# Kernel tuning notes

Hardware: AMD Instinct MI355X
Metric: run time of the kernel (lower is better)

Reference implementation:

```python
import jax, jax.numpy as jnp
import numpy as np

B, N, E = 8, 4096, 8190
V, H, OUT = 256, 128, 128


def setup_inputs() -> dict:
    key = jax.random.key(0)
    ks = jax.random.split(key, 7)
    return {
        "type_ids": jax.random.randint(ks[0], (B, N), 0, V),
        "edges": jax.random.randint(ks[1], (B, E, 2), 0, N),
        "emb": jax.random.normal(ks[2], (V, H), jnp.float32) * 0.02,
        "w1": jax.random.normal(ks[3], (H, H), jnp.float32) * (1.0 / np.sqrt(H)),
        "b1": jax.random.normal(ks[4], (H,), jnp.float32) * 0.01,
        "w2": jax.random.normal(ks[5], (OUT, H), jnp.float32) * (1.0 / np.sqrt(H)),
        "b2": jax.random.normal(ks[6], (OUT,), jnp.float32) * 0.01,
    }


def reference(type_ids, edges, emb, w1, b1, w2, b2):
    # X: [B, N, H] embedded node types
    X = emb[type_ids]
    b_idx = jnp.broadcast_to(jnp.arange(type_ids.shape[0])[:, None], edges.shape[:2])
    # dense adjacency, set (not add) like torch adj[i, j] = 1.0; then + I
    adj = jnp.zeros((type_ids.shape[0], N, N), X.dtype)
    adj = adj.at[b_idx, edges[..., 0], edges[..., 1]].set(1.0)
    adj = adj + jnp.eye(N, dtype=X.dtype)
    # symmetric degree normalization: A = D^-1/2 (adj) D^-1/2
    deg = adj.sum(axis=-1)
    dis = jnp.maximum(deg, 1.0) ** -0.5  # deg.clamp(min=1.0) ** -0.5
    A = dis[:, :, None] * adj * dis[:, None, :]
    # two-layer GCN (torch Linear: x @ W.T + b)
    h = jax.nn.relu(jnp.einsum("bnm,bmh->bnh", A, X) @ w1.T + b1)
    z = jnp.einsum("bnm,bmh->bnh", A, h) @ w2.T + b2
    zbar = z.mean(axis=1)  # per-graph mean pool -> [B, OUT]
    # F.normalize(dim=-1), eps=1e-12
    norm = jnp.maximum(jnp.linalg.norm(zbar, axis=-1, keepdims=True), 1e-12)
    return zbar / norm
```

## Files before the change

### kernel.cpp

```cpp
#include <hip/hip_runtime.h>
#include <hip/hip_bf16.h>
#include <stdint.h>

#define BB 8
#define NN 4096
#define NE 8190
#define VV 256
#define HH 128
#define WPR 64
#define MAXD 32
#define SLICES 64
#define RPB 8

__global__ void k_scatter(const int* __restrict__ edges,
                          unsigned long long* __restrict__ bits,
                          int* __restrict__ outdeg, int* __restrict__ indeg,
                          unsigned short* __restrict__ outl,
                          unsigned short* __restrict__ inl) {
    int idx = blockIdx.x * blockDim.x + threadIdx.x;
    if (idx >= BB * NE) return;
    int b = idx / NE;
    int src = edges[idx * 2 + 0];
    int dst = edges[idx * 2 + 1];
    int row = b * NN + src;
    unsigned long long m = 1ull << (dst & 63);
    unsigned long long old = atomicOr(&bits[(size_t)row * WPR + (dst >> 6)], m);
    if (!(old & m)) {
        int po = atomicAdd(&outdeg[row], 1);
        if (po < MAXD) outl[(size_t)row * MAXD + po] = (unsigned short)dst;
        int col = b * NN + dst;
        int pi = atomicAdd(&indeg[col], 1);
        if (pi < MAXD) inl[(size_t)col * MAXD + pi] = (unsigned short)src;
    }
}

__global__ void k_embw1(const float* __restrict__ emb,
                        const float* __restrict__ w1,
                        float* __restrict__ embw1) {
    __shared__ float er[HH];
    int v = blockIdx.x, o = threadIdx.x;
    er[o] = emb[v * HH + o];
    __syncthreads();
    float acc = 0.f;
#pragma unroll 8
    for (int k = 0; k < HH; k++) acc += er[k] * w1[o * HH + k];
    embw1[v * HH + o] = acc;
}

__global__ void k_fused(const int* __restrict__ type_ids,
                        const float* __restrict__ embw1,
                        const int* __restrict__ outdeg,
                        const int* __restrict__ indeg,
                        const unsigned short* __restrict__ outl,
                        const unsigned short* __restrict__ inl,
                        const float* __restrict__ b1,
                        float* __restrict__ p) {
    __shared__ float djs[MAXD];
    __shared__ int   tjs[MAXD];
    __shared__ float s_sh;
    int t = threadIdx.x;
    int blk = blockIdx.x;
    int base = blk * RPB;
    int b = base >> 12;
    float b1t = b1[t];
    float psum = 0.f;

    for (int r = 0; r < RPB; r++) {
        int row = base + r;
        int mo = min(outdeg[row], MAXD);
        int mi = min(indeg[row], MAXD);
        if (t < mo) {
            int gj = b * NN + (int)outl[(size_t)row * MAXD + t];
            djs[t] = rsqrtf((float)(outdeg[gj] + 1));
            tjs[t] = type_ids[gj];
        }
        float sloc = 0.f;
        if (t < mi) {
            int gu = b * NN + (int)inl[(size_t)row * MAXD + t];
            sloc = rsqrtf((float)(outdeg[gu] + 1));
        }
        if (t < 64) {
#pragma unroll
            for (int off = 16; off >= 1; off >>= 1)
                sloc += __shfl_down(sloc, off, 32);
            if (t == 0) s_sh = sloc;
        }
        __syncthreads();
        float dis_i = rsqrtf((float)(outdeg[row] + 1));
        int ti = type_ids[row];
        float acc = dis_i * embw1[ti * HH + t];
        for (int q = 0; q < mo; q++)
            acc += djs[q] * embw1[tjs[q] * HH + t];
        float h = fmaxf(dis_i * acc + b1t, 0.f);
        float c = dis_i * (s_sh + dis_i);
        psum += c * h;
        __syncthreads();
    }
    int slice = blk & (SLICES - 1);
    atomicAdd(&p[((size_t)b * SLICES + slice) * HH + t], psum);
}

__global__ void k_final(const float* __restrict__ p,
                        const float* __restrict__ w2,
                        const float* __restrict__ b2,
                        float* __restrict__ out) {
    __shared__ float pl[HH];
    __shared__ float red[HH];
    int b = blockIdx.x, o = threadIdx.x;
    float accp = 0.f;
#pragma unroll 8
    for (int sct = 0; sct < SLICES; sct++)
        accp += p[((size_t)b * SLICES + sct) * HH + o];
    pl[o] = accp * (1.0f / (float)NN);
    __syncthreads();
    float acc = b2[o];
#pragma unroll 8
    for (int k = 0; k < HH; k++) acc += pl[k] * w2[o * HH + k];
    red[o] = acc * acc;
    __syncthreads();
    for (int stride = 64; stride > 0; stride >>= 1) {
        if (o < stride) red[o] += red[o + stride];
        __syncthreads();
    }
    float denom = fmaxf(sqrtf(red[0]), 1e-12f);
    out[b * HH + o] = acc / denom;
}

extern "C" void kernel_launch(void* const* d_in, const int* in_sizes, int n_in,
                              void* d_out, int out_size, void* d_ws, size_t ws_size,
                              hipStream_t stream) {
    const int*   type_ids = (const int*)d_in[0];
    const int*   edges    = (const int*)d_in[1];
    const float* emb      = (const float*)d_in[2];
    const float* w1       = (const float*)d_in[3];
    const float* b1       = (const float*)d_in[4];
    const float* w2       = (const float*)d_in[5];
    const float* b2       = (const float*)d_in[6];
    float* out = (float*)d_out;

    char* ws = (char*)d_ws;
    unsigned long long* bits = (unsigned long long*)ws;
    size_t off = (size_t)BB * NN * WPR * 8;
    int* outdeg = (int*)(ws + off);          off += (size_t)BB * NN * 4;
    int* indeg  = (int*)(ws + off);          off += (size_t)BB * NN * 4;
    float* p    = (float*)(ws + off);        off += (size_t)BB * SLICES * HH * 4;
    size_t zero_bytes = off;
    unsigned short* outl = (unsigned short*)(ws + off); off += (size_t)BB * NN * MAXD * 2;
    unsigned short* inl  = (unsigned short*)(ws + off); off += (size_t)BB * NN * MAXD * 2;
    float* embw1 = (float*)(ws + off);

    hipMemsetAsync(ws, 0, zero_bytes, stream);

    k_scatter<<<(BB * NE + 255) / 256, 256, 0, stream>>>(edges, bits, outdeg,
                                                         indeg, outl, inl);
    k_embw1<<<VV, HH, 0, stream>>>(emb, w1, embw1);
    k_fused<<<BB * NN / RPB, HH, 0, stream>>>(type_ids, embw1, outdeg, indeg,
                                              outl, inl, b1, p);
    k_final<<<BB, HH, 0, stream>>>(p, w2, b2, out);
}
```

Measured before the change: 110.4 us.

## Replace dense adjacency bitmap with deferred duplicate-edge filtering on neighbor lists

Drops the per-graph 64-bit adjacency bitmap, which needed a large workspace memset and random atomicOr traffic during the edge scatter. Out- and in-degrees are now counted raw into one interleaved array. Duplicate edges are removed later by pairwise comparison within each node's short neighbor list, both in a new precompute kernel (which also builds per-node normalisation/type metadata) and inside the fused kernel. The embedding-times-W1 precompute is merged into the same launch, and the partial-sum slice count is halved. In exchange, the fused kernel does extra quadratic comparisons per row. Lists still hold at most MAXD entries, but duplicates now use up that capacity before they are filtered out.

```diff
diff --git a/kernel.cpp b/kernel.cpp
--- a/kernel.cpp
+++ b/kernel.cpp
@@ -7,14 +7,12 @@
 #define NE 8190
 #define VV 256
 #define HH 128
-#define WPR 64
 #define MAXD 32
-#define SLICES 64
+#define SLICES 32
 #define RPB 8
 
 __global__ void k_scatter(const int* __restrict__ edges,
-                          unsigned long long* __restrict__ bits,
-                          int* __restrict__ outdeg, int* __restrict__ indeg,
+                          int* __restrict__ deg,
                           unsigned short* __restrict__ outl,
                           unsigned short* __restrict__ inl) {
     int idx = blockIdx.x * blockDim.x + threadIdx.x;
@@ -23,38 +21,58 @@
     int src = edges[idx * 2 + 0];
     int dst = edges[idx * 2 + 1];
     int row = b * NN + src;
-    unsigned long long m = 1ull << (dst & 63);
-    unsigned long long old = atomicOr(&bits[(size_t)row * WPR + (dst >> 6)], m);
-    if (!(old & m)) {
-        int po = atomicAdd(&outdeg[row], 1);
-        if (po < MAXD) outl[(size_t)row * MAXD + po] = (unsigned short)dst;
-        int col = b * NN + dst;
-        int pi = atomicAdd(&indeg[col], 1);
-        if (pi < MAXD) inl[(size_t)col * MAXD + pi] = (unsigned short)src;
+    int col = b * NN + dst;
+    int po = atomicAdd(&deg[2 * row + 0], 1);
+    if (po < MAXD) outl[(size_t)row * MAXD + po] = (unsigned short)dst;
+    int pi = atomicAdd(&deg[2 * col + 1], 1);
+    if (pi < MAXD) inl[(size_t)col * MAXD + pi] = (unsigned short)src;
+}
+
+__global__ void k_meta_embw1(const int* __restrict__ type_ids,
+                             const int* __restrict__ deg,
+                             const unsigned short* __restrict__ outl,
+                             const float* __restrict__ emb,
+                             const float* __restrict__ w1,
+                             float2* __restrict__ meta,
+                             float* __restrict__ embw1) {
+    int blk = blockIdx.x, t = threadIdx.x;
+    if (blk < 128) {
+        int row = blk * 256 + t;
+        int raw = min(deg[2 * row], MAXD);
+        unsigned short c[MAXD];
+        for (int k = 0; k < raw; k++) c[k] = outl[(size_t)row * MAXD + k];
+        int uniq = 0;
+        for (int k = 0; k < raw; k++) {
+            bool dup = false;
+            for (int j = 0; j < k; j++) dup |= (c[j] == c[k]);
+            uniq += dup ? 0 : 1;
+        }
+        float2 m;
+        m.x = rsqrtf((float)(uniq + 1));
+        m.y = __int_as_float(type_ids[row]);
+        meta[row] = m;
+    } else {
+        __shared__ float er[256];
+        int v = (blk - 128) * 2 + (t >> 7);
+        int o = t & 127;
+        er[t] = emb[v * HH + o];
+        __syncthreads();
+        const float* erow = &er[(t >> 7) * HH];
+        float acc = 0.f;
+#pragma unroll 8
+        for (int k = 0; k < HH; k++) acc += erow[k] * w1[o * HH + k];
+        embw1[v * HH + o] = acc;
     }
 }
 
-__global__ void k_embw1(const float* __restrict__ emb,
-                        const float* __restrict__ w1,
-                        float* __restrict__ embw1) {
-    __shared__ float er[HH];
-    int v = blockIdx.x, o = threadIdx.x;
-    er[o] = emb[v * HH + o];
-    __syncthreads();
-    float acc = 0.f;
-#pragma unroll 8
-    for (int k = 0; k < HH; k++) acc += er[k] * w1[o * HH + k];
-    embw1[v * HH + o] = acc;
-}
-
-__global__ void k_fused(const int* __restrict__ type_ids,
+__global__ void k_fused(const float2* __restrict__ meta,
                         const float* __restrict__ embw1,
-                        const int* __restrict__ outdeg,
-                        const int* __restrict__ indeg,
+                        const int* __restrict__ deg,
                         const unsigned short* __restrict__ outl,
                         const unsigned short* __restrict__ inl,
                         const float* __restrict__ b1,
                         float* __restrict__ p) {
+    __shared__ unsigned short colso[MAXD], colsi[MAXD];
     __shared__ float djs[MAXD];
     __shared__ int   tjs[MAXD];
     __shared__ float s_sh;
@@ -67,17 +85,25 @@
 
     for (int r = 0; r < RPB; r++) {
         int row = base + r;
-        int mo = min(outdeg[row], MAXD);
-        int mi = min(indeg[row], MAXD);
-        if (t < mo) {
-            int gj = b * NN + (int)outl[(size_t)row * MAXD + t];
-            djs[t] = rsqrtf((float)(outdeg[gj] + 1));
-            tjs[t] = type_ids[gj];
+        int rawo = min(deg[2 * row + 0], MAXD);
+        int rawi = min(deg[2 * row + 1], MAXD);
+        if (t < rawo) colso[t] = outl[(size_t)row * MAXD + t];
+        if (t < rawi) colsi[t] = inl[(size_t)row * MAXD + t];
+        __syncthreads();
+        if (t < rawo) {
+            unsigned short cc = colso[t];
+            bool dup = false;
+            for (int j = 0; j < t; j++) dup |= (colso[j] == cc);
+            float2 m = meta[b * NN + cc];
+            djs[t] = dup ? 0.f : m.x;
+            tjs[t] = __float_as_int(m.y);
         }
         float sloc = 0.f;
-        if (t < mi) {
-            int gu = b * NN + (int)inl[(size_t)row * MAXD + t];
-            sloc = rsqrtf((float)(outdeg[gu] + 1));
+        if (t < rawi) {
+            unsigned short cc = colsi[t];
+            bool dup = false;
+            for (int j = 0; j < t; j++) dup |= (colsi[j] == cc);
+            sloc = dup ? 0.f : meta[b * NN + cc].x;
         }
         if (t < 64) {
 #pragma unroll
@@ -86,14 +112,13 @@
             if (t == 0) s_sh = sloc;
         }
         __syncthreads();
-        float dis_i = rsqrtf((float)(outdeg[row] + 1));
-        int ti = type_ids[row];
-        float acc = dis_i * embw1[ti * HH + t];
-        for (int q = 0; q < mo; q++)
+        float2 mi = meta[row];
+        float dis_i = mi.x;
+        float acc = dis_i * embw1[__float_as_int(mi.y) * HH + t];
+        for (int q = 0; q < rawo; q++)
             acc += djs[q] * embw1[tjs[q] * HH + t];
         float h = fmaxf(dis_i * acc + b1t, 0.f);
-        float c = dis_i * (s_sh + dis_i);
-        psum += c * h;
+        psum += dis_i * (s_sh + dis_i) * h;
         __syncthreads();
     }
     int slice = blk & (SLICES - 1);
@@ -139,22 +164,19 @@
     float* out = (float*)d_out;
 
     char* ws = (char*)d_ws;
-    unsigned long long* bits = (unsigned long long*)ws;
-    size_t off = (size_t)BB * NN * WPR * 8;
-    int* outdeg = (int*)(ws + off);          off += (size_t)BB * NN * 4;
-    int* indeg  = (int*)(ws + off);          off += (size_t)BB * NN * 4;
-    float* p    = (float*)(ws + off);        off += (size_t)BB * SLICES * HH * 4;
+    int* deg = (int*)ws;
+    size_t off = (size_t)BB * NN * 2 * 4;
+    float* p = (float*)(ws + off); off += (size_t)BB * SLICES * HH * 4;
     size_t zero_bytes = off;
     unsigned short* outl = (unsigned short*)(ws + off); off += (size_t)BB * NN * MAXD * 2;
     unsigned short* inl  = (unsigned short*)(ws + off); off += (size_t)BB * NN * MAXD * 2;
+    float2* meta = (float2*)(ws + off); off += (size_t)BB * NN * 8;
     float* embw1 = (float*)(ws + off);
 
     hipMemsetAsync(ws, 0, zero_bytes, stream);
 
-    k_scatter<<<(BB * NE + 255) / 256, 256, 0, stream>>>(edges, bits, outdeg,
-                                                         indeg, outl, inl);
-    k_embw1<<<VV, HH, 0, stream>>>(emb, w1, embw1);
-    k_fused<<<BB * NN / RPB, HH, 0, stream>>>(type_ids, embw1, outdeg, indeg,
-                                              outl, inl, b1, p);
+    k_scatter<<<(BB * NE + 255) / 256, 256, 0, stream>>>(edges, deg, outl, inl);
+    k_meta_embw1<<<384, 256, 0, stream>>>(type_ids, deg, outl, emb, w1, meta, embw1);
+    k_fused<<<BB * NN / RPB, HH, 0, stream>>>(meta, embw1, deg, outl, inl, b1, p);
     k_final<<<BB, HH, 0, stream>>>(p, w2, b2, out);
 }
```

After: 139.5 us. 1.26x slower.

## Merge scatter with embW1 and fold final pooling into last fused block

Applied to the files above, without the earlier changes.

Combines the edge scatter and emb@W1 precompute into one launch using block-index branching. The final projection and normalization move into the fused kernel's last-finishing block, found through an atomic counter with threadfences. The out and in degree arrays are interleaved as int2, each block's adjacency lists are staged in shared memory, and the partial-sum slices drop from 64 to 16. This removes two kernel launches and some scattered global reads, but adds more atomic contention on fewer slices and a serial tail in the one finishing block.

```diff
diff --git a/kernel.cpp b/kernel.cpp
--- a/kernel.cpp
+++ b/kernel.cpp
@@ -9,75 +9,94 @@
 #define HH 128
 #define WPR 64
 #define MAXD 32
-#define SLICES 64
+#define SLICES 16
 #define RPB 8
+#define NBLK_FUSED (BB * NN / RPB)
 
-__global__ void k_scatter(const int* __restrict__ edges,
-                          unsigned long long* __restrict__ bits,
-                          int* __restrict__ outdeg, int* __restrict__ indeg,
-                          unsigned short* __restrict__ outl,
-                          unsigned short* __restrict__ inl) {
-    int idx = blockIdx.x * blockDim.x + threadIdx.x;
-    if (idx >= BB * NE) return;
-    int b = idx / NE;
-    int src = edges[idx * 2 + 0];
-    int dst = edges[idx * 2 + 1];
-    int row = b * NN + src;
-    unsigned long long m = 1ull << (dst & 63);
-    unsigned long long old = atomicOr(&bits[(size_t)row * WPR + (dst >> 6)], m);
-    if (!(old & m)) {
-        int po = atomicAdd(&outdeg[row], 1);
-        if (po < MAXD) outl[(size_t)row * MAXD + po] = (unsigned short)dst;
-        int col = b * NN + dst;
-        int pi = atomicAdd(&indeg[col], 1);
-        if (pi < MAXD) inl[(size_t)col * MAXD + pi] = (unsigned short)src;
+__global__ void k_scatter_embw1(const int* __restrict__ edges,
+                                const float* __restrict__ emb,
+                                const float* __restrict__ w1,
+                                unsigned long long* __restrict__ bits,
+                                int2* __restrict__ deg,
+                                unsigned short* __restrict__ outl,
+                                unsigned short* __restrict__ inl,
+                                float* __restrict__ embw1) {
+    int blk = blockIdx.x, t = threadIdx.x;
+    if (blk < 256) {
+        int idx = blk * 256 + t;
+        if (idx >= BB * NE) return;
+        int b = idx / NE;
+        int src = edges[idx * 2 + 0];
+        int dst = edges[idx * 2 + 1];
+        int row = b * NN + src;
+        unsigned long long m = 1ull << (dst & 63);
+        unsigned long long old = atomicOr(&bits[(size_t)row * WPR + (dst >> 6)], m);
+        if (!(old & m)) {
+            int po = atomicAdd(&deg[row].x, 1);
+            if (po < MAXD) outl[(size_t)row * MAXD + po] = (unsigned short)dst;
+            int col = b * NN + dst;
+            int pi = atomicAdd(&deg[col].y, 1);
+            if (pi < MAXD) inl[(size_t)col * MAXD + pi] = (unsigned short)src;
+        }
+    } else {
+        __shared__ float er[256];
+        int v = (blk - 256) * 2 + (t >> 7);
+        int o = t & 127;
+        er[t] = emb[v * HH + o];
+        __syncthreads();
+        const float* erow = &er[(t >> 7) * HH];
+        float acc = 0.f;
+#pragma unroll 8
+        for (int k = 0; k < HH; k++) acc += erow[k] * w1[o * HH + k];
+        embw1[v * HH + o] = acc;
     }
 }
 
-__global__ void k_embw1(const float* __restrict__ emb,
-                        const float* __restrict__ w1,
-                        float* __restrict__ embw1) {
-    __shared__ float er[HH];
-    int v = blockIdx.x, o = threadIdx.x;
-    er[o] = emb[v * HH + o];
-    __syncthreads();
-    float acc = 0.f;
-#pragma unroll 8
-    for (int k = 0; k < HH; k++) acc += er[k] * w1[o * HH + k];
-    embw1[v * HH + o] = acc;
-}
-
-__global__ void k_fused(const int* __restrict__ type_ids,
-                        const float* __restrict__ embw1,
-                        const int* __restrict__ outdeg,
-                        const int* __restrict__ indeg,
-                        const unsigned short* __restrict__ outl,
-                        const unsigned short* __restrict__ inl,
-                        const float* __restrict__ b1,
-                        float* __restrict__ p) {
+__global__ void __launch_bounds__(128)
+k_fused(const int* __restrict__ type_ids,
+        const float* __restrict__ embw1,
+        const int2* __restrict__ deg,
+        const unsigned short* __restrict__ outl,
+        const unsigned short* __restrict__ inl,
+        const float* __restrict__ b1,
+        const float* __restrict__ w2,
+        const float* __restrict__ b2,
+        float* __restrict__ p,
+        int* __restrict__ cnt,
+        float* __restrict__ out) {
+    __shared__ unsigned short colsO[RPB][MAXD];
+    __shared__ unsigned short colsI[RPB][MAXD];
+    __shared__ int2  degsh[RPB];
+    __shared__ int   tidsh[RPB];
     __shared__ float djs[MAXD];
     __shared__ int   tjs[MAXD];
     __shared__ float s_sh;
+    __shared__ int   lastsh;
+
     int t = threadIdx.x;
     int blk = blockIdx.x;
     int base = blk * RPB;
     int b = base >> 12;
+
+    ((unsigned int*)colsO)[t] = ((const unsigned int*)(outl + (size_t)base * MAXD))[t];
+    ((unsigned int*)colsI)[t] = ((const unsigned int*)(inl  + (size_t)base * MAXD))[t];
+    if (t < RPB) { degsh[t] = deg[base + t]; tidsh[t] = type_ids[base + t]; }
     float b1t = b1[t];
+    __syncthreads();
+
     float psum = 0.f;
-
     for (int r = 0; r < RPB; r++) {
-        int row = base + r;
-        int mo = min(outdeg[row], MAXD);
-        int mi = min(indeg[row], MAXD);
+        int mo = min(degsh[r].x, MAXD);
+        int mi = min(degsh[r].y, MAXD);
         if (t < mo) {
-            int gj = b * NN + (int)outl[(size_t)row * MAXD + t];
-            djs[t] = rsqrtf((float)(outdeg[gj] + 1));
+            int gj = b * NN + (int)colsO[r][t];
+            djs[t] = rsqrtf((float)(deg[gj].x + 1));
             tjs[t] = type_ids[gj];
         }
         float sloc = 0.f;
         if (t < mi) {
-            int gu = b * NN + (int)inl[(size_t)row * MAXD + t];
-            sloc = rsqrtf((float)(outdeg[gu] + 1));
+            int gu = b * NN + (int)colsI[r][t];
+            sloc = rsqrtf((float)(deg[gu].x + 1));
         }
         if (t < 64) {
 #pragma unroll
@@ -86,44 +105,54 @@
             if (t == 0) s_sh = sloc;
         }
         __syncthreads();
-        float dis_i = rsqrtf((float)(outdeg[row] + 1));
-        int ti = type_ids[row];
-        float acc = dis_i * embw1[ti * HH + t];
+        float dis_i = rsqrtf((float)(degsh[r].x + 1));
+        float acc = dis_i * embw1[tidsh[r] * HH + t];
         for (int q = 0; q < mo; q++)
             acc += djs[q] * embw1[tjs[q] * HH + t];
         float h = fmaxf(dis_i * acc + b1t, 0.f);
-        float c = dis_i * (s_sh + dis_i);
-        psum += c * h;
+        psum += dis_i * (s_sh + dis_i) * h;
         __syncthreads();
     }
     int slice = blk & (SLICES - 1);
     atomicAdd(&p[((size_t)b * SLICES + slice) * HH + t], psum);
-}
 
-__global__ void k_final(const float* __restrict__ p,
-                        const float* __restrict__ w2,
-                        const float* __restrict__ b2,
-                        float* __restrict__ out) {
-    __shared__ float pl[HH];
-    __shared__ float red[HH];
-    int b = blockIdx.x, o = threadIdx.x;
-    float accp = 0.f;
-#pragma unroll 8
-    for (int sct = 0; sct < SLICES; sct++)
-        accp += p[((size_t)b * SLICES + sct) * HH + o];
-    pl[o] = accp * (1.0f / (float)NN);
+    __threadfence();
+    if (t == 0) lastsh = atomicAdd(cnt, 1);
     __syncthreads();
-    float acc = b2[o];
-#pragma unroll 8
-    for (int k = 0; k < HH; k++) acc += pl[k] * w2[o * HH + k];
-    red[o] = acc * acc;
+    if (lastsh != NBLK_FUSED - 1) return;
+    __threadfence();
+
+    __shared__ float pl[BB][HH];
+    __shared__ float red[BB][HH];
+    for (int bb = 0; bb < BB; bb++) {
+        float accp = 0.f;
+#pragma unroll
+        for (int s = 0; s < SLICES; s++)
+            accp += p[((size_t)bb * SLICES + s) * HH + t];
+        pl[bb][t] = accp * (1.0f / (float)NN);
+    }
+    __syncthreads();
+    float accb[BB];
+#pragma unroll
+    for (int bb = 0; bb < BB; bb++) accb[bb] = b2[t];
+    for (int k = 0; k < HH; k++) {
+        float wv = w2[t * HH + k];
+#pragma unroll
+        for (int bb = 0; bb < BB; bb++) accb[bb] += pl[bb][k] * wv;
+    }
+#pragma unroll
+    for (int bb = 0; bb < BB; bb++) red[bb][t] = accb[bb] * accb[bb];
     __syncthreads();
     for (int stride = 64; stride > 0; stride >>= 1) {
-        if (o < stride) red[o] += red[o + stride];
+        if (t < stride) {
+#pragma unroll
+            for (int bb = 0; bb < BB; bb++) red[bb][t] += red[bb][t + stride];
+        }
         __syncthreads();
     }
-    float denom = fmaxf(sqrtf(red[0]), 1e-12f);
-    out[b * HH + o] = acc / denom;
+#pragma unroll
+    for (int bb = 0; bb < BB; bb++)
+        out[bb * HH + t] = accb[bb] / fmaxf(sqrtf(red[bb][0]), 1e-12f);
 }
 
 extern "C" void kernel_launch(void* const* d_in, const int* in_sizes, int n_in,
@@ -141,20 +170,17 @@
     char* ws = (char*)d_ws;
     unsigned long long* bits = (unsigned long long*)ws;
     size_t off = (size_t)BB * NN * WPR * 8;
-    int* outdeg = (int*)(ws + off);          off += (size_t)BB * NN * 4;
-    int* indeg  = (int*)(ws + off);          off += (size_t)BB * NN * 4;
-    float* p    = (float*)(ws + off);        off += (size_t)BB * SLICES * HH * 4;
+    int2* deg = (int2*)(ws + off);   off += (size_t)BB * NN * 8;
+    float* p  = (float*)(ws + off);  off += (size_t)BB * SLICES * HH * 4;
+    int* cnt  = (int*)(ws + off);    off += 128;
     size_t zero_bytes = off;
     unsigned short* outl = (unsigned short*)(ws + off); off += (size_t)BB * NN * MAXD * 2;
     unsigned short* inl  = (unsigned short*)(ws + off); off += (size_t)BB * NN * MAXD * 2;
     float* embw1 = (float*)(ws + off);
 
     hipMemsetAsync(ws, 0, zero_bytes, stream);
-
-    k_scatter<<<(BB * NE + 255) / 256, 256, 0, stream>>>(edges, bits, outdeg,
-                                                         indeg, outl, inl);
-    k_embw1<<<VV, HH, 0, stream>>>(emb, w1, embw1);
-    k_fused<<<BB * NN / RPB, HH, 0, stream>>>(type_ids, embw1, outdeg, indeg,
-                                              outl, inl, b1, p);
-    k_final<<<BB, HH, 0, stream>>>(p, w2, b2, out);
+    k_scatter_embw1<<<384, 256, 0, stream>>>(edges, emb, w1, bits, deg,
+                                             outl, inl, embw1);
+    k_fused<<<NBLK_FUSED, 128, 0, stream>>>(type_ids, embw1, deg, outl, inl,
+                                            b1, w2, b2, p, cnt, out);
 }
```

Result: slower. 243.7 us (+120.7%).

## Fuse edge scatter with embedding projection kernel and interleave degree arrays

Applied to the files above, without the earlier changes.

Merges the edge-scatter and emb@W1 kernels into one launch, with blocks split by index into scatter work and two-row projection work, which removes a kernel launch and lets the two run concurrently. Out-degree and in-degree are packed into one int2 array so a single load fetches both, and partial-sum slices are halved. The __launch_bounds__ hint and fewer slices trade more atomic contention on p for a smaller memset and a shorter final reduction.

```diff
diff --git a/kernel.cpp b/kernel.cpp
--- a/kernel.cpp
+++ b/kernel.cpp
@@ -9,52 +9,56 @@
 #define HH 128
 #define WPR 64
 #define MAXD 32
-#define SLICES 64
+#define SLICES 32
 #define RPB 8
 
-__global__ void k_scatter(const int* __restrict__ edges,
-                          unsigned long long* __restrict__ bits,
-                          int* __restrict__ outdeg, int* __restrict__ indeg,
-                          unsigned short* __restrict__ outl,
-                          unsigned short* __restrict__ inl) {
-    int idx = blockIdx.x * blockDim.x + threadIdx.x;
-    if (idx >= BB * NE) return;
-    int b = idx / NE;
-    int src = edges[idx * 2 + 0];
-    int dst = edges[idx * 2 + 1];
-    int row = b * NN + src;
-    unsigned long long m = 1ull << (dst & 63);
-    unsigned long long old = atomicOr(&bits[(size_t)row * WPR + (dst >> 6)], m);
-    if (!(old & m)) {
-        int po = atomicAdd(&outdeg[row], 1);
-        if (po < MAXD) outl[(size_t)row * MAXD + po] = (unsigned short)dst;
-        int col = b * NN + dst;
-        int pi = atomicAdd(&indeg[col], 1);
-        if (pi < MAXD) inl[(size_t)col * MAXD + pi] = (unsigned short)src;
+__global__ void k_scatter_embw1(const int* __restrict__ edges,
+                                const float* __restrict__ emb,
+                                const float* __restrict__ w1,
+                                unsigned long long* __restrict__ bits,
+                                int2* __restrict__ deg,
+                                unsigned short* __restrict__ outl,
+                                unsigned short* __restrict__ inl,
+                                float* __restrict__ embw1) {
+    int blk = blockIdx.x, t = threadIdx.x;
+    if (blk < 256) {
+        int idx = blk * 256 + t;
+        if (idx >= BB * NE) return;
+        int b = idx / NE;
+        int src = edges[idx * 2 + 0];
+        int dst = edges[idx * 2 + 1];
+        int row = b * NN + src;
+        unsigned long long m = 1ull << (dst & 63);
+        unsigned long long old = atomicOr(&bits[(size_t)row * WPR + (dst >> 6)], m);
+        if (!(old & m)) {
+            int po = atomicAdd(&deg[row].x, 1);
+            if (po < MAXD) outl[(size_t)row * MAXD + po] = (unsigned short)dst;
+            int col = b * NN + dst;
+            int pi = atomicAdd(&deg[col].y, 1);
+            if (pi < MAXD) inl[(size_t)col * MAXD + pi] = (unsigned short)src;
+        }
+    } else {
+        __shared__ float er[256];
+        int v = (blk - 256) * 2 + (t >> 7);
+        int o = t & 127;
+        er[t] = emb[v * HH + o];
+        __syncthreads();
+        const float* erow = &er[(t >> 7) * HH];
+        float acc = 0.f;
+#pragma unroll 8
+        for (int k = 0; k < HH; k++) acc += erow[k] * w1[o * HH + k];
+        embw1[v * HH + o] = acc;
     }
 }
 
-__global__ void k_embw1(const float* __restrict__ emb,
-                        const float* __restrict__ w1,
-                        float* __restrict__ embw1) {
-    __shared__ float er[HH];
-    int v = blockIdx.x, o = threadIdx.x;
-    er[o] = emb[v * HH + o];
-    __syncthreads();
-    float acc = 0.f;
-#pragma unroll 8
-    for (int k = 0; k < HH; k++) acc += er[k] * w1[o * HH + k];
-    embw1[v * HH + o] = acc;
-}
-
-__global__ void k_fused(const int* __restrict__ type_ids,
-                        const float* __restrict__ embw1,
-                        const int* __restrict__ outdeg,
-                        const int* __restrict__ indeg,
-                        const unsigned short* __restrict__ outl,
-                        const unsigned short* __restrict__ inl,
-                        const float* __restrict__ b1,
-                        float* __restrict__ p) {
+__global__ void __launch_bounds__(128)
+k_fused(const int* __restrict__ type_ids,
+        const float* __restrict__ embw1,
+        const int2* __restrict__ deg,
+        const unsigned short* __restrict__ outl,
+        const unsigned short* __restrict__ inl,
+        const float* __restrict__ b1,
+        float* __restrict__ p) {
     __shared__ float djs[MAXD];
     __shared__ int   tjs[MAXD];
     __shared__ float s_sh;
@@ -67,17 +71,18 @@
 
     for (int r = 0; r < RPB; r++) {
         int row = base + r;
-        int mo = min(outdeg[row], MAXD);
-        int mi = min(indeg[row], MAXD);
+        int2 dg = deg[row];
+        int mo = min(dg.x, MAXD);
+        int mi = min(dg.y, MAXD);
         if (t < mo) {
             int gj = b * NN + (int)outl[(size_t)row * MAXD + t];
-            djs[t] = rsqrtf((float)(outdeg[gj] + 1));
+            djs[t] = rsqrtf((float)(deg[gj].x + 1));
             tjs[t] = type_ids[gj];
         }
         float sloc = 0.f;
         if (t < mi) {
             int gu = b * NN + (int)inl[(size_t)row * MAXD + t];
-            sloc = rsqrtf((float)(outdeg[gu] + 1));
+            sloc = rsqrtf((float)(deg[gu].x + 1));
         }
         if (t < 64) {
 #pragma unroll
@@ -86,14 +91,12 @@
             if (t == 0) s_sh = sloc;
         }
         __syncthreads();
-        float dis_i = rsqrtf((float)(outdeg[row] + 1));
-        int ti = type_ids[row];
-        float acc = dis_i * embw1[ti * HH + t];
+        float dis_i = rsqrtf((float)(dg.x + 1));
+        float acc = dis_i * embw1[type_ids[row] * HH + t];
         for (int q = 0; q < mo; q++)
             acc += djs[q] * embw1[tjs[q] * HH + t];
         float h = fmaxf(dis_i * acc + b1t, 0.f);
-        float c = dis_i * (s_sh + dis_i);
-        psum += c * h;
+        psum += dis_i * (s_sh + dis_i) * h;
         __syncthreads();
     }
     int slice = blk & (SLICES - 1);
@@ -141,20 +144,17 @@
     char* ws = (char*)d_ws;
     unsigned long long* bits = (unsigned long long*)ws;
     size_t off = (size_t)BB * NN * WPR * 8;
-    int* outdeg = (int*)(ws + off);          off += (size_t)BB * NN * 4;
-    int* indeg  = (int*)(ws + off);          off += (size_t)BB * NN * 4;
-    float* p    = (float*)(ws + off);        off += (size_t)BB * SLICES * HH * 4;
+    int2* deg = (int2*)(ws + off);   off += (size_t)BB * NN * 8;
+    float* p  = (float*)(ws + off);  off += (size_t)BB * SLICES * HH * 4;
     size_t zero_bytes = off;
     unsigned short* outl = (unsigned short*)(ws + off); off += (size_t)BB * NN * MAXD * 2;
     unsigned short* inl  = (unsigned short*)(ws + off); off += (size_t)BB * NN * MAXD * 2;
     float* embw1 = (float*)(ws + off);
 
     hipMemsetAsync(ws, 0, zero_bytes, stream);
-
-    k_scatter<<<(BB * NE + 255) / 256, 256, 0, stream>>>(edges, bits, outdeg,
-                                                         indeg, outl, inl);
-    k_embw1<<<VV, HH, 0, stream>>>(emb, w1, embw1);
-    k_fused<<<BB * NN / RPB, HH, 0, stream>>>(type_ids, embw1, outdeg, indeg,
-                                              outl, inl, b1, p);
+    k_scatter_embw1<<<384, 256, 0, stream>>>(edges, emb, w1, bits, deg,
+                                             outl, inl, embw1);
+    k_fused<<<BB * NN / RPB, 128, 0, stream>>>(type_ids, embw1, deg, outl, inl,
+                                               b1, p);
     k_final<<<BB, HH, 0, stream>>>(p, w2, b2, out);
 }
```

After: 107.5 us. 2.7% less time.
